# Performance work log

Hardware: AMD Instinct MI355X
Metric: run time of the kernel (lower is better)

The kernel has to match this reference:

```python
import jax, jax.numpy as jnp
import numpy as np

N, D, K = 65536, 256, 4096
EPS = 1e-5
DECAY = 0.99
BN_MOMENTUM = 0.1


def setup_inputs() -> dict:
    key = jax.random.key(0)
    k1, k2, k3, k4, k5, k6 = jax.random.split(key, 6)
    return {
        "x": jax.random.normal(k1, (N, D), dtype=jnp.float32),
        "embedding": jax.random.normal(k2, (K, D), dtype=jnp.float32),
        "ema_cluster_size": jnp.zeros((K,), dtype=jnp.float32),
        "ema_w": jax.random.normal(k3, (K, D), dtype=jnp.float32),
        "running_mean": jax.random.normal(k4, (D,), dtype=jnp.float32) * 0.1,
        "running_var": jax.random.uniform(k5, (D,), dtype=jnp.float32, minval=0.5, maxval=1.5),
    }


def reference(x, embedding, ema_cluster_size, ema_w, running_mean, running_var):
    n_batch = x.shape[0]
    num_embeddings = embedding.shape[0]

    # BatchNorm1d (training mode, affine=False): normalize with batch stats
    mean = jnp.mean(x, axis=0)                       # [D]
    var = jnp.mean((x - mean) ** 2, axis=0)          # biased var, [D]
    xn = (x - mean) / jnp.sqrt(var + EPS)            # [N, D]
    # running stat updates (torch uses unbiased var for running_var)
    new_running_mean = (1.0 - BN_MOMENTUM) * running_mean + BN_MOMENTUM * mean
    var_unbiased = var * (n_batch / (n_batch - 1.0))
    new_running_var = (1.0 - BN_MOMENTUM) * running_var + BN_MOMENTUM * var_unbiased

    # squared euclidean distances [N, K]
    distances = (jnp.sum(xn ** 2, axis=1, keepdims=True)
                 + jnp.sum(embedding ** 2, axis=1)
                 - 2.0 * xn @ embedding.T)
    idx = jnp.argmin(distances, axis=1)              # [N]

    # one-hot scatter stats via segment_sum (== encodings.T contractions)
    counts = jax.ops.segment_sum(jnp.ones((n_batch,), dtype=x.dtype), idx,
                                 num_segments=num_embeddings)   # [K]
    dw = jax.ops.segment_sum(xn, idx, num_segments=num_embeddings)  # [K, D]

    # EMA updates
    new_cs = ema_cluster_size * DECAY + (1.0 - DECAY) * counts
    n_total = jnp.sum(new_cs)
    new_cs = (new_cs + 1e-5) / (n_total + num_embeddings * 1e-5) * n_total
    new_ema_w = ema_w * DECAY + (1.0 - DECAY) * dw
    new_embedding = new_ema_w / new_cs[:, None]

    running_std = jnp.sqrt(new_running_var + EPS)
    embedding_output = new_embedding * running_std[None, :] + new_running_mean[None, :]

    return (idx[:, None], new_embedding, embedding_output, new_cs, new_ema_w,
            new_running_mean, new_running_var)
```

## Files before the change

kernel.cpp:

```cpp
#include <hip/hip_runtime.h>
#include <cfloat>
#include <cmath>

#define NROWS 65536
#define DDIM 256
#define KDIM 4096

typedef short bf16x8 __attribute__((ext_vector_type(8)));
typedef float f32x4 __attribute__((ext_vector_type(4)));

constexpr float EPSV = 1e-5f;
constexpr float DECAYV = 0.99f;
constexpr float MOMV = 0.1f;
constexpr float DELTA = 0.5f;
constexpr int CAP = 16;
constexpr int SEG = 128;

constexpr size_t WS_CNT     = 0;
constexpr size_t WS_NFLAG   = WS_CNT + NROWS;
constexpr size_t WS_HIST    = WS_NFLAG + 64;
constexpr size_t WS_START   = WS_HIST + KDIM;
constexpr size_t WS_FILLPOS = WS_START + KDIM;
constexpr size_t WS_SEGSTART= WS_FILLPOS + KDIM;
constexpr size_t WS_NSEG    = WS_SEGSTART + KDIM + 64;
constexpr size_t WS_SEGLIST = WS_NSEG + 64;
constexpr size_t WS_PARTSUM = WS_SEGLIST + 4672;
constexpr size_t WS_PARTSQ  = WS_PARTSUM + 512 * DDIM;
constexpr size_t WS_MEAN    = WS_PARTSQ + 512 * DDIM;
constexpr size_t WS_RSTD    = WS_MEAN + DDIM;
constexpr size_t WS_NRMEAN  = WS_RSTD + DDIM;
constexpr size_t WS_NRVAR   = WS_NRMEAN + DDIM;
constexpr size_t WS_BVEC    = WS_NRVAR + DDIM;
constexpr size_t WS_NCSRAW  = WS_BVEC + KDIM;
constexpr size_t WS_NTOT    = WS_NCSRAW + KDIM;
constexpr size_t WS_ROWINFO = WS_NTOT + 64;
constexpr size_t WS_IDX     = WS_ROWINFO + 8 * (size_t)NROWS;
constexpr size_t WS_ROWTHR  = WS_IDX + NROWS;
constexpr size_t WS_FLAG    = WS_ROWTHR + NROWS;
constexpr size_t WS_ROWLIST = WS_FLAG + NROWS;
constexpr size_t WS_CAND    = WS_ROWLIST + NROWS;
constexpr size_t WS_DWPART  = WS_CAND;
constexpr size_t WS_EPROW   = WS_CAND + (size_t)NROWS * CAP;
constexpr size_t WS_EIMG    = WS_EPROW + (size_t)KDIM * DDIM;
constexpr size_t WS_XIMG    = WS_EIMG + 524288;

constexpr size_t O_IDX   = 0;
constexpr size_t O_EMB   = NROWS;
constexpr size_t O_EOUT  = O_EMB + (size_t)KDIM * DDIM;
constexpr size_t O_CS    = O_EOUT + (size_t)KDIM * DDIM;
constexpr size_t O_EMAW  = O_CS + KDIM;
constexpr size_t O_RMEAN = O_EMAW + (size_t)KDIM * DDIM;
constexpr size_t O_RVAR  = O_RMEAN + DDIM;

__device__ inline unsigned bfpack(float a, float b) {
    unsigned ua = __float_as_uint(a), ub = __float_as_uint(b);
    ua = (ua + 0x7FFFu + ((ua >> 16) & 1u)) >> 16;
    ub = (ub + 0x7FFFu + ((ub >> 16) & 1u)) & 0xFFFF0000u;
    return (ua & 0xFFFFu) | ub;
}

__device__ inline float unpackval(float p) {
    return __uint_as_float(__float_as_uint(p) & 0xFFFFF000u);
}

#define GLOAD_LDS16(g, l) __builtin_amdgcn_global_load_lds(                       \
        (const __attribute__((address_space(1))) void*)(g),                        \
        (__attribute__((address_space(3))) void*)(l), 16, 0, 0)

__global__ __launch_bounds__(256) void k_bnpack(const float* __restrict__ x,
                                                float* __restrict__ ws) {
    __shared__ float4 lsum[4][64], lsq[4][64];
    const int t = threadIdx.x;
    const int gid = blockIdx.x * 256 + t;
    if (gid < NROWS) ((int*)(ws + WS_CNT))[gid] = 0;
    if (gid < KDIM) ((int*)(ws + WS_HIST))[gid] = 0;
    if (gid == 0) *(int*)(ws + WS_NFLAG) = 0;
    const int q = t & 63, g = t >> 6;
    const int r0 = blockIdx.x * 128 + g * 32;
    char* ximg = (char*)(ws + WS_XIMG);
    const float4* x4 = (const float4*)x;
    float4 s = make_float4(0.f, 0.f, 0.f, 0.f);
    float4 sq = make_float4(0.f, 0.f, 0.f, 0.f);
#pragma unroll 4
    for (int i = 0; i < 32; ++i) {
        const int r = r0 + i;
        const float4 v = x4[(size_t)r * 64 + q];
        s.x += v.x; s.y += v.y; s.z += v.z; s.w += v.w;
        sq.x += v.x * v.x; sq.y += v.y * v.y; sq.z += v.z * v.z; sq.w += v.w * v.w;
        const int db = (8 * q + ((r & 15) << 5)) & 511;
        *(uint2*)(ximg + (size_t)r * 512 + db) = make_uint2(bfpack(v.x, v.y), bfpack(v.z, v.w));
    }
    lsum[g][q] = s; lsq[g][q] = sq;
    __syncthreads();
    if (t < 64) {
        const float4 a0 = lsum[0][t], a1 = lsum[1][t], a2 = lsum[2][t], a3 = lsum[3][t];
        const float4 b0 = lsq[0][t],  b1 = lsq[1][t],  b2 = lsq[2][t],  b3 = lsq[3][t];
        float4 S, Q;
        S.x = (a0.x + a1.x) + (a2.x + a3.x); S.y = (a0.y + a1.y) + (a2.y + a3.y);
        S.z = (a0.z + a1.z) + (a2.z + a3.z); S.w = (a0.w + a1.w) + (a2.w + a3.w);
        Q.x = (b0.x + b1.x) + (b2.x + b3.x); Q.y = (b0.y + b1.y) + (b2.y + b3.y);
        Q.z = (b0.z + b1.z) + (b2.z + b3.z); Q.w = (b0.w + b1.w) + (b2.w + b3.w);
        ((float4*)(ws + WS_PARTSUM))[(size_t)blockIdx.x * 64 + t] = S;
        ((float4*)(ws + WS_PARTSQ))[(size_t)blockIdx.x * 64 + t]  = Q;
    }
}

__global__ __launch_bounds__(256) void k_bn_final(const float* __restrict__ rmean_in,
                                                  const float* __restrict__ rvar_in,
                                                  float* __restrict__ ws,
                                                  float* __restrict__ out) {
    const int d = threadIdx.x;
    float s = 0.f, sq = 0.f;
    for (int b = 0; b < 512; ++b) {
        s  += ws[WS_PARTSUM + (size_t)b * DDIM + d];
        sq += ws[WS_PARTSQ  + (size_t)b * DDIM + d];
    }
    const float mean = s / (float)NROWS;
    float var = sq / (float)NROWS - mean * mean;
    var = fmaxf(var, 0.f);
    const float rstd = 1.0f / sqrtf(var + EPSV);
    const float nrm  = (1.0f - MOMV) * rmean_in[d] + MOMV * mean;
    const float varu = var * ((float)NROWS / (float)(NROWS - 1));
    const float nrv  = (1.0f - MOMV) * rvar_in[d] + MOMV * varu;
    ws[WS_MEAN + d] = mean;
    ws[WS_RSTD + d] = rstd;
    ws[WS_NRMEAN + d] = nrm;
    ws[WS_NRVAR + d] = nrv;
    out[O_RMEAN + d] = nrm;
    out[O_RVAR + d] = nrv;
}

__global__ __launch_bounds__(256) void k_eprime(const float* __restrict__ emb,
                                                float* __restrict__ ws) {
    const int t = threadIdx.x, l = t & 63, w = t >> 6;
    const int k = blockIdx.x * 4 + w;
    const float4 em = ((const float4*)emb)[(size_t)k * 64 + l];
    const float4 rs = ((const float4*)(ws + WS_RSTD))[l];
    const float4 mn = ((const float4*)(ws + WS_MEAN))[l];
    float4 e;
    e.x = em.x * rs.x; e.y = em.y * rs.y; e.z = em.z * rs.z; e.w = em.w * rs.w;
    ((float4*)(ws + WS_EPROW))[(size_t)k * 64 + l] = e;
    char* img = (char*)(ws + WS_EIMG);
    const int db = (8 * l + ((k & 15) << 5)) & 511;
    *(uint2*)(img + (size_t)k * 512 + db) =
        make_uint2(bfpack(-2.f * e.x, -2.f * e.y), bfpack(-2.f * e.z, -2.f * e.w));
    float red = em.x * em.x + 2.f * mn.x * e.x + em.y * em.y + 2.f * mn.y * e.y
              + em.z * em.z + 2.f * mn.z * e.z + em.w * em.w + 2.f * mn.w * e.w;
    red += __shfl_xor(red, 32); red += __shfl_xor(red, 16); red += __shfl_xor(red, 8);
    red += __shfl_xor(red, 4);  red += __shfl_xor(red, 2);  red += __shfl_xor(red, 1);
    if (l == 0) ws[WS_BVEC + k] = red;
}

__global__ __launch_bounds__(256, 4) void k_gemm_min(float* __restrict__ ws) {
    extern __shared__ char smem[];
    const int t = threadIdx.x, lane = t & 63, w = t >> 6;
    const int l4 = lane & 15, kg = lane >> 4;
    const int tile = blockIdx.x >> 2;
    const int cq   = blockIdx.x & 3;
    const int rowbase = tile * 128 + w * 32;
    const char* ximg = (const char*)(ws + WS_XIMG);
    const char* eimg = (const char*)(ws + WS_EIMG) + (size_t)cq * 524288;
    const float* bvec = ws + WS_BVEC;

    bf16x8 a[2][8];
#pragma unroll
    for (int m = 0; m < 2; ++m) {
        const char* rp = ximg + (size_t)(rowbase + m * 16 + l4) * 512;
#pragma unroll
        for (int ts = 0; ts < 8; ++ts) {
            const int byte = ((kg * 16 + ts * 64) + (l4 << 5)) & 511;
            a[m][ts] = *(const bf16x8*)(rp + byte);
        }
    }

    float b1f[2][4], b2f[2][4];
#pragma unroll
    for (int m = 0; m < 2; ++m)
#pragma unroll
        for (int r = 0; r < 4; ++r) { b1f[m][r] = FLT_MAX; b2f[m][r] = FLT_MAX; }

#pragma unroll
    for (int rr = 0; rr < 4; ++rr) {
        const int off = rr * 4096 + w * 1024;
        GLOAD_LDS16(eimg + off + lane * 16, smem + off);
    }
    float bc0 = bvec[cq * 1024 + l4];
    float bc1 = bvec[cq * 1024 + 16 + l4];
    __syncthreads();

    for (int ch = 0; ch < 32; ++ch) {
        const char* cur = smem + (ch & 1) * 16384;
        float bn0 = 0.f, bn1 = 0.f;
        if (ch + 1 < 32) {
            const char* src = eimg + (size_t)(ch + 1) * 16384;
            char* nb = smem + ((ch + 1) & 1) * 16384;
#pragma unroll
            for (int rr = 0; rr < 4; ++rr) {
                const int off = rr * 4096 + w * 1024;
                GLOAD_LDS16(src + off + lane * 16, nb + off);
            }
            bn0 = bvec[cq * 1024 + (ch + 1) * 32 + l4];
            bn1 = bvec[cq * 1024 + (ch + 1) * 32 + 16 + l4];
        }

        f32x4 acc[2][2];
        acc[0][0] = (f32x4){bc0, bc0, bc0, bc0};
        acc[0][1] = (f32x4){bc1, bc1, bc1, bc1};
        acc[1][0] = acc[0][0];
        acc[1][1] = acc[0][1];

#pragma unroll
        for (int ts = 0; ts < 8; ++ts) {
            const int rot = ((kg * 16 + ts * 64) + (l4 << 5)) & 511;
            bf16x8 bfr[2];
#pragma unroll
            for (int n = 0; n < 2; ++n)
                bfr[n] = *(const bf16x8*)(cur + (n * 16 + l4) * 512 + rot);
#pragma unroll
            for (int m = 0; m < 2; ++m)
#pragma unroll
                for (int n = 0; n < 2; ++n)
                    acc[m][n] = __builtin_amdgcn_mfma_f32_16x16x32_bf16(a[m][ts], bfr[n], acc[m][n], 0, 0, 0);
        }

#pragma unroll
        for (int n = 0; n < 2; ++n) {
            const unsigned col = (unsigned)(cq * 1024 + ch * 32 + n * 16 + l4);
#pragma unroll
            for (int m = 0; m < 2; ++m)
#pragma unroll
                for (int r = 0; r < 4; ++r) {
                    const float p = __uint_as_float(
                        (__float_as_uint(acc[m][n][r]) & 0xFFFFF000u) | col);
                    b2f[m][r] = __builtin_amdgcn_fmed3f(p, b1f[m][r], b2f[m][r]);
                    b1f[m][r] = fminf(p, b1f[m][r]);
                }
        }
        bc0 = bn0; bc1 = bn1;
        __syncthreads();
    }

    float2* rowinfo = (float2*)(ws + WS_ROWINFO);
#pragma unroll
    for (int m = 0; m < 2; ++m)
#pragma unroll
        for (int r = 0; r < 4; ++r) {
            float v1 = b1f[m][r], v2 = b2f[m][r];
#pragma unroll
            for (int st = 1; st < 16; st <<= 1) {
                const float o1 = __shfl_xor(v1, st);
                const float o2 = __shfl_xor(v2, st);
                const float mm = fminf(v2, o2);
                v2 = __builtin_amdgcn_fmed3f(v1, o1, mm);
                v1 = fminf(v1, o1);
            }
            if (l4 == 0) {
                const int row = rowbase + m * 16 + kg * 4 + r;
                rowinfo[(size_t)row * 4 + cq] = make_float2(v1, v2);
            }
        }
}

__global__ __launch_bounds__(256) void k_flag(float* __restrict__ ws,
                                              float* __restrict__ out) {
    const int r = blockIdx.x * 256 + threadIdx.x;
    const float2* rowinfo = (const float2*)(ws + WS_ROWINFO);
    float2 q = rowinfo[(size_t)r * 4];
    float v1 = q.x, v2 = q.y;
#pragma unroll
    for (int c = 1; c < 4; ++c) {
        q = rowinfo[(size_t)r * 4 + c];
        const float mm = fminf(v2, q.y);
        v2 = __builtin_amdgcn_fmed3f(v1, q.x, mm);
        v1 = fminf(v1, q.x);
    }
    const float v1v = unpackval(v1);
    const int   i1  = (int)(__float_as_uint(v1) & 0xFFFu);
    ws[WS_ROWTHR + r] = v1v + DELTA;
    if (unpackval(v2) - v1v <= DELTA) {
        const int pos = atomicAdd((int*)(ws + WS_NFLAG), 1);
        ((int*)(ws + WS_FLAG))[pos] = r;
    } else {
        out[O_IDX + r] = (float)i1;
        ((int*)(ws + WS_IDX))[r] = i1;
        atomicAdd((int*)(ws + WS_HIST) + i1, 1);
    }
}

__global__ __launch_bounds__(256) void k_cand(float* __restrict__ ws) {
    extern __shared__ char smem[];
    const int t = threadIdx.x, lane = t & 63, w = t >> 6;
    const int l4 = lane & 15, kg = lane >> 4;
    const char* ximg = (const char*)(ws + WS_XIMG);
    const char* eimg0 = (const char*)(ws + WS_EIMG);
    const float* bvec = ws + WS_BVEC;
    const int* flag = (const int*)(ws + WS_FLAG);
    int* cnt = (int*)(ws + WS_CNT);
    int* cand = (int*)(ws + WS_CAND);
    const int nflag = *(const int*)(ws + WS_NFLAG);
    if (nflag == 0) return;
    const int ntiles = (nflag + 127) >> 7;
    const int nitems = ntiles * 8;

    for (int item = blockIdx.x; item < nitems; item += gridDim.x) {
        const int tile = item >> 3, slice = item & 7;
        const int base = tile * 128 + w * 32;
        const char* eimg = eimg0 + (size_t)slice * 262144;
        bf16x8 a[2][8];
        int frow[2][4];
        float thr[2][4];
#pragma unroll
        for (int m = 0; m < 2; ++m) {
            const int ia = base + m * 16 + l4;
            const int rowa = flag[ia < nflag ? ia : (nflag - 1)];
            const char* rp = ximg + (size_t)rowa * 512;
#pragma unroll
            for (int ts = 0; ts < 8; ++ts) {
                const int byte = ((kg * 16 + ts * 64) + ((rowa & 15) << 5)) & 511;
                a[m][ts] = *(const bf16x8*)(rp + byte);
            }
#pragma unroll
            for (int r = 0; r < 4; ++r) {
                const int ie = base + m * 16 + kg * 4 + r;
                const bool val = ie < nflag;
                const int rowe = flag[val ? ie : (nflag - 1)];
                frow[m][r] = rowe;
                thr[m][r] = val ? ws[WS_ROWTHR + rowe] : -FLT_MAX;
            }
        }
#pragma unroll
        for (int rr = 0; rr < 4; ++rr) {
            const int off = rr * 4096 + w * 1024;
            GLOAD_LDS16(eimg + off + lane * 16, smem + off);
        }
        __syncthreads();

        for (int ch = 0; ch < 16; ++ch) {
            const char* cur = smem + (ch & 1) * 16384;
            if (ch + 1 < 16) {
                const char* src = eimg + (size_t)(ch + 1) * 16384;
                char* nb = smem + ((ch + 1) & 1) * 16384;
#pragma unroll
                for (int rr = 0; rr < 4; ++rr) {
                    const int off = rr * 4096 + w * 1024;
                    GLOAD_LDS16(src + off + lane * 16, nb + off);
                }
            }
            const float bc0 = bvec[slice * 512 + ch * 32 + l4];
            const float bc1 = bvec[slice * 512 + ch * 32 + 16 + l4];
            f32x4 acc[2][2];
            acc[0][0] = (f32x4){bc0, bc0, bc0, bc0};
            acc[0][1] = (f32x4){bc1, bc1, bc1, bc1};
            acc[1][0] = acc[0][0];
            acc[1][1] = acc[0][1];
#pragma unroll
            for (int ts = 0; ts < 8; ++ts) {
                const int rot = ((kg * 16 + ts * 64) + (l4 << 5)) & 511;
                bf16x8 bfr[2];
#pragma unroll
                for (int n = 0; n < 2; ++n)
                    bfr[n] = *(const bf16x8*)(cur + (n * 16 + l4) * 512 + rot);
#pragma unroll
                for (int m = 0; m < 2; ++m)
#pragma unroll
                    for (int n = 0; n < 2; ++n)
                        acc[m][n] = __builtin_amdgcn_mfma_f32_16x16x32_bf16(a[m][ts], bfr[n], acc[m][n], 0, 0, 0);
            }
#pragma unroll
            for (int n = 0; n < 2; ++n) {
                const int col = slice * 512 + ch * 32 + n * 16 + l4;
#pragma unroll
                for (int m = 0; m < 2; ++m)
#pragma unroll
                    for (int r = 0; r < 4; ++r) {
                        const float s = acc[m][n][r];
                        if (s <= thr[m][r]) {
                            const int rr2 = frow[m][r];
                            const int pos = atomicAdd(&cnt[rr2], 1);
                            if (pos < CAP) cand[(size_t)rr2 * CAP + pos] = col;
                        }
                    }
            }
            __syncthreads();
        }
    }
}

__global__ __launch_bounds__(256) void k_resolve_f(const float* __restrict__ x,
                                                   float* __restrict__ ws,
                                                   float* __restrict__ out) {
    const int t = threadIdx.x, lane = t & 63;
    const int gw = (blockIdx.x * 256 + t) >> 6;
    const int nflag = *(const int*)(ws + WS_NFLAG);
    const int* flag = (const int*)(ws + WS_FLAG);
    const int* cnt = (const int*)(ws + WS_CNT);
    const int* cand = (const int*)(ws + WS_CAND);
    const float* eprow = ws + WS_EPROW;
    const float* bvec = ws + WS_BVEC;
    int* idx_int = (int*)(ws + WS_IDX);
    for (int i = gw; i < nflag; i += 1024) {
        const int row = flag[i];
        const float4 xr = ((const float4*)(x + (size_t)row * DDIM))[lane];
        const int n = cnt[row];
        float bestv = FLT_MAX;
        int bestk = KDIM;
        if (n >= 1 && n <= CAP) {
            for (int c = 0; c < n; ++c) {
                const int k = cand[(size_t)row * CAP + c];
                const float4 er = ((const float4*)(eprow + (size_t)k * DDIM))[lane];
                float p = xr.x * er.x + xr.y * er.y + xr.z * er.z + xr.w * er.w;
                p += __shfl_xor(p, 32); p += __shfl_xor(p, 16); p += __shfl_xor(p, 8);
                p += __shfl_xor(p, 4);  p += __shfl_xor(p, 2);  p += __shfl_xor(p, 1);
                const float s = fmaf(-2.f, p, bvec[k]);
                if (s < bestv || (s == bestv && k < bestk)) { bestv = s; bestk = k; }
            }
        } else {
            for (int k = 0; k < KDIM; ++k) {
                const float4 er = ((const float4*)(eprow + (size_t)k * DDIM))[lane];
                float p = xr.x * er.x + xr.y * er.y + xr.z * er.z + xr.w * er.w;
                p += __shfl_xor(p, 32); p += __shfl_xor(p, 16); p += __shfl_xor(p, 8);
                p += __shfl_xor(p, 4);  p += __shfl_xor(p, 2);  p += __shfl_xor(p, 1);
                const float s = fmaf(-2.f, p, bvec[k]);
                if (s < bestv || (s == bestv && k < bestk)) { bestv = s; bestk = k; }
            }
        }
        if (lane == 0) {
            out[O_IDX + row] = (float)bestk;
            idx_int[row] = bestk;
            atomicAdd((int*)(ws + WS_HIST) + bestk, 1);
        }
    }
}

__global__ __launch_bounds__(256) void k_scan(const float* __restrict__ cs_in,
                                              float* __restrict__ ws) {
    __shared__ int lsum[256], lseg[256];
    __shared__ float redf[256];
    const int t = threadIdx.x;
    const int* hist = (const int*)(ws + WS_HIST);
    int h[16];
    int s = 0, g = 0;
#pragma unroll
    for (int i = 0; i < 16; ++i) {
        h[i] = hist[t * 16 + i];
        s += h[i];
        g += (h[i] + SEG - 1) / SEG;
    }
    lsum[t] = s; lseg[t] = g;
    __syncthreads();
    int v = s, u = g;
    for (int off = 1; off < 256; off <<= 1) {
        const int av = (t >= off) ? lsum[t - off] : 0;
        const int au = (t >= off) ? lseg[t - off] : 0;
        __syncthreads();
        v += av; u += au;
        lsum[t] = v; lseg[t] = u;
        __syncthreads();
    }
    int runs = v - s, rung = u - g;
    int* start = (int*)(ws + WS_START);
    int* fillpos = (int*)(ws + WS_FILLPOS);
    int* segst = (int*)(ws + WS_SEGSTART);
    int* seglist = (int*)(ws + WS_SEGLIST);
    float emapart = 0.f;
#pragma unroll
    for (int i = 0; i < 16; ++i) {
        const int k = t * 16 + i;
        start[k] = runs;
        fillpos[k] = runs;
        segst[k] = rung;
        const int ns = (h[i] + SEG - 1) / SEG;
        for (int j = 0; j < ns; ++j) seglist[rung + j] = (k << 10) | j;
        runs += h[i];
        rung += ns;
        const float ncs = cs_in[k] * DECAYV + (1.0f - DECAYV) * (float)h[i];
        ws[WS_NCSRAW + k] = ncs;
        emapart += ncs;
    }
    if (t == 255) {
        segst[KDIM] = rung;
        *(int*)(ws + WS_NSEG) = rung;
    }
    redf[t] = emapart;
    __syncthreads();
    for (int ss = 128; ss > 0; ss >>= 1) { if (t < ss) redf[t] += redf[t + ss]; __syncthreads(); }
    if (t == 0) ws[WS_NTOT] = redf[0];
}

__global__ __launch_bounds__(256) void k_fill(float* __restrict__ ws) {
    const int r = blockIdx.x * 256 + threadIdx.x;
    const int k = ((const int*)(ws + WS_IDX))[r];
    const int pos = atomicAdd((int*)(ws + WS_FILLPOS) + k, 1);
    ((int*)(ws + WS_ROWLIST))[pos] = r;
}

__global__ __launch_bounds__(256) void k_gather_seg(const float* __restrict__ x,
                                                    float* __restrict__ ws) {
    __shared__ float4 ls[4][64];
    const int b = blockIdx.x;
    if (b >= *(const int*)(ws + WS_NSEG)) return;
    const int e = ((const int*)(ws + WS_SEGLIST))[b];
    const int k = e >> 10, j = e & 1023;
    const int base = ((const int*)(ws + WS_START))[k];
    const int n = ((const int*)(ws + WS_HIST))[k];
    const int st = base + j * SEG;
    const int en = min(st + SEG, base + n);
    const int* rowlist = (const int*)(ws + WS_ROWLIST);
    const int t = threadIdx.x, q = t & 63, g = t >> 6;
    const float4* x4 = (const float4*)x;
    float4 s = make_float4(0.f, 0.f, 0.f, 0.f);
    for (int i = st + g; i < en; i += 4) {
        const float4 v = x4[(size_t)rowlist[i] * 64 + q];
        s.x += v.x; s.y += v.y; s.z += v.z; s.w += v.w;
    }
    ls[g][q] = s;
    __syncthreads();
    if (t < 64) {
        const float4 a0 = ls[0][t], a1 = ls[1][t], a2 = ls[2][t], a3 = ls[3][t];
        float4 r;
        r.x = (a0.x + a1.x) + (a2.x + a3.x);
        r.y = (a0.y + a1.y) + (a2.y + a3.y);
        r.z = (a0.z + a1.z) + (a2.z + a3.z);
        r.w = (a0.w + a1.w) + (a2.w + a3.w);
        ((float4*)(ws + WS_DWPART))[(size_t)b * 64 + t] = r;
    }
}

__global__ __launch_bounds__(64) void k_final(const float* __restrict__ ema_w,
                                              const float* __restrict__ ws,
                                              float* __restrict__ out) {
    const int k = blockIdx.x;
    const int q = threadIdx.x;
    const int* segst = (const int*)(ws + WS_SEGSTART);
    const int ss = segst[k];
    const int ns = segst[k + 1] - ss;
    const float4* dwpart = (const float4*)(ws + WS_DWPART);
    float4 a = make_float4(0.f, 0.f, 0.f, 0.f);
    for (int j = 0; j < ns; ++j) {
        const float4 v = dwpart[(size_t)(ss + j) * 64 + q];
        a.x += v.x; a.y += v.y; a.z += v.z; a.w += v.w;
    }
    const int n = ((const int*)(ws + WS_HIST))[k];
    const float ntot = ws[WS_NTOT];
    const float ncs  = (ws[WS_NCSRAW + k] + 1e-5f) / (ntot + (float)KDIM * 1e-5f) * ntot;
    const float4 mn = ((const float4*)(ws + WS_MEAN))[q];
    const float4 rs = ((const float4*)(ws + WS_RSTD))[q];
    const float4 nrv = ((const float4*)(ws + WS_NRVAR))[q];
    const float4 nrm = ((const float4*)(ws + WS_NRMEAN))[q];
    const float4 ew = ((const float4*)ema_w)[(size_t)k * 64 + q];
    const float fn = (float)n;
    float4 nwv, nembv, eov;
    nwv.x = ew.x * DECAYV + (1.f - DECAYV) * ((a.x - fn * mn.x) * rs.x);
    nwv.y = ew.y * DECAYV + (1.f - DECAYV) * ((a.y - fn * mn.y) * rs.y);
    nwv.z = ew.z * DECAYV + (1.f - DECAYV) * ((a.z - fn * mn.z) * rs.z);
    nwv.w = ew.w * DECAYV + (1.f - DECAYV) * ((a.w - fn * mn.w) * rs.w);
    const float inv = 1.0f / ncs;
    nembv.x = nwv.x * inv; nembv.y = nwv.y * inv;
    nembv.z = nwv.z * inv; nembv.w = nwv.w * inv;
    eov.x = nembv.x * sqrtf(nrv.x + EPSV) + nrm.x;
    eov.y = nembv.y * sqrtf(nrv.y + EPSV) + nrm.y;
    eov.z = nembv.z * sqrtf(nrv.z + EPSV) + nrm.z;
    eov.w = nembv.w * sqrtf(nrv.w + EPSV) + nrm.w;
    ((float4*)(out + O_EMB))[(size_t)k * 64 + q]  = nembv;
    ((float4*)(out + O_EOUT))[(size_t)k * 64 + q] = eov;
    ((float4*)(out + O_EMAW))[(size_t)k * 64 + q] = nwv;
    if (q == 0) out[O_CS + k] = ncs;
}

extern "C" void kernel_launch(void* const* d_in, const int* in_sizes, int n_in,
                              void* d_out, int out_size, void* d_ws, size_t ws_size,
                              hipStream_t stream) {
    const float* x     = (const float*)d_in[0];
    const float* emb   = (const float*)d_in[1];
    const float* cs    = (const float*)d_in[2];
    const float* ema_w = (const float*)d_in[3];
    const float* rmean = (const float*)d_in[4];
    const float* rvar  = (const float*)d_in[5];
    float* out = (float*)d_out;
    float* ws  = (float*)d_ws;

    k_bnpack<<<512, 256, 0, stream>>>(x, ws);
    k_bn_final<<<1, 256, 0, stream>>>(rmean, rvar, ws, out);
    k_eprime<<<KDIM / 4, 256, 0, stream>>>(emb, ws);

    constexpr int LDSB = 32768;
    k_gemm_min<<<2048, 256, LDSB, stream>>>(ws);
    k_flag<<<NROWS / 256, 256, 0, stream>>>(ws, out);
    k_cand<<<512, 256, LDSB, stream>>>(ws);
    k_resolve_f<<<256, 256, 0, stream>>>(x, ws, out);

    k_scan<<<1, 256, 0, stream>>>(cs, ws);
    k_fill<<<NROWS / 256, 256, 0, stream>>>(ws);
    k_gather_seg<<<4608, 256, 0, stream>>>(x, ws);
    k_final<<<KDIM, 64, 0, stream>>>(ema_w, ws, out);
}
```

Baseline: 312.6 us.

## Triple-buffer codebook chunks in GEMM-argmin with explicit vmcnt waits

Turns the double-buffered LDS prefetch of codebook chunks in the distance/argmin GEMM into a three-stage ring. Fine-grained s_waitcnt vmcnt plus raw barriers let two chunks stay in flight while the current one is computed. The per-column bias vector is staged once into LDS instead of being loaded from global memory every iteration. In exchange, LDS use grows to about 52KB and launch bounds drop to 3 blocks per CU, which may reduce occupancy.

```diff
diff --git a/kernel.cpp b/kernel.cpp
--- a/kernel.cpp
+++ b/kernel.cpp
@@ -151,8 +151,9 @@
     if (l == 0) ws[WS_BVEC + k] = red;
 }
 
-__global__ __launch_bounds__(256, 4) void k_gemm_min(float* __restrict__ ws) {
+__global__ __launch_bounds__(256, 3) void k_gemm_min(float* __restrict__ ws) {
     extern __shared__ char smem[];
+    float* bls = (float*)(smem + 49152);
     const int t = threadIdx.x, lane = t & 63, w = t >> 6;
     const int l4 = lane & 15, kg = lane >> 4;
     const int tile = blockIdx.x >> 2;
@@ -162,6 +163,8 @@
     const char* eimg = (const char*)(ws + WS_EIMG) + (size_t)cq * 524288;
     const float* bvec = ws + WS_BVEC;
 
+    ((float4*)bls)[t] = ((const float4*)(bvec + cq * 1024))[t];
+
     bf16x8 a[2][8];
 #pragma unroll
     for (int m = 0; m < 2; ++m) {
@@ -180,28 +183,37 @@
         for (int r = 0; r < 4; ++r) { b1f[m][r] = FLT_MAX; b2f[m][r] = FLT_MAX; }
 
 #pragma unroll
-    for (int rr = 0; rr < 4; ++rr) {
-        const int off = rr * 4096 + w * 1024;
-        GLOAD_LDS16(eimg + off + lane * 16, smem + off);
-    }
-    float bc0 = bvec[cq * 1024 + l4];
-    float bc1 = bvec[cq * 1024 + 16 + l4];
+    for (int c0 = 0; c0 < 2; ++c0)
+#pragma unroll
+        for (int rr = 0; rr < 4; ++rr) {
+            const int off = rr * 4096 + w * 1024;
+            GLOAD_LDS16(eimg + (size_t)c0 * 16384 + off + lane * 16,
+                        smem + c0 * 16384 + off);
+        }
     __syncthreads();
 
+    int cb = 0, sb = 2;
     for (int ch = 0; ch < 32; ++ch) {
-        const char* cur = smem + (ch & 1) * 16384;
-        float bn0 = 0.f, bn1 = 0.f;
-        if (ch + 1 < 32) {
-            const char* src = eimg + (size_t)(ch + 1) * 16384;
-            char* nb = smem + ((ch + 1) & 1) * 16384;
+        if (ch + 2 < 32) {
+            const char* src = eimg + (size_t)(ch + 2) * 16384;
+            char* nb = smem + sb * 16384;
 #pragma unroll
             for (int rr = 0; rr < 4; ++rr) {
                 const int off = rr * 4096 + w * 1024;
                 GLOAD_LDS16(src + off + lane * 16, nb + off);
             }
-            bn0 = bvec[cq * 1024 + (ch + 1) * 32 + l4];
-            bn1 = bvec[cq * 1024 + (ch + 1) * 32 + 16 + l4];
-        }
+            asm volatile("s_waitcnt vmcnt(8)" ::: "memory");
+        } else if (ch + 1 < 32) {
+            asm volatile("s_waitcnt vmcnt(4)" ::: "memory");
+        } else {
+            asm volatile("s_waitcnt vmcnt(0)" ::: "memory");
+        }
+        __builtin_amdgcn_sched_barrier(0);
+        __builtin_amdgcn_s_barrier();
+
+        const char* cur = smem + cb * 16384;
+        const float bc0 = bls[ch * 32 + l4];
+        const float bc1 = bls[ch * 32 + 16 + l4];
 
         f32x4 acc[2][2];
         acc[0][0] = (f32x4){bc0, bc0, bc0, bc0};
@@ -236,8 +248,9 @@
                     b1f[m][r] = fminf(p, b1f[m][r]);
                 }
         }
-        bc0 = bn0; bc1 = bn1;
-        __syncthreads();
+        __builtin_amdgcn_s_barrier();
+        cb = (cb == 2) ? 0 : cb + 1;
+        sb = (sb == 2) ? 0 : sb + 1;
     }
 
     float2* rowinfo = (float2*)(ws + WS_ROWINFO);
@@ -583,10 +596,11 @@
     k_bn_final<<<1, 256, 0, stream>>>(rmean, rvar, ws, out);
     k_eprime<<<KDIM / 4, 256, 0, stream>>>(emb, ws);
 
-    constexpr int LDSB = 32768;
-    k_gemm_min<<<2048, 256, LDSB, stream>>>(ws);
+    constexpr int LDSB_G = 3 * 16384 + 4096;
+    constexpr int LDSB_C = 32768;
+    k_gemm_min<<<2048, 256, LDSB_G, stream>>>(ws);
     k_flag<<<NROWS / 256, 256, 0, stream>>>(ws, out);
-    k_cand<<<512, 256, LDSB, stream>>>(ws);
+    k_cand<<<512, 256, LDSB_C, stream>>>(ws);
     k_resolve_f<<<256, 256, 0, stream>>>(x, ws, out);
 
     k_scan<<<1, 256, 0, stream>>>(cs, ws);
```

Result: no change. 316.1 us (+1.1%).
